# Optimization experiments

Measured on AMD Instinct MI355X. Metric: run time of the kernel, lower is better.

## Reference

```python
import jax, jax.numpy as jnp
import numpy as np

DIM = 384; H = 56; W = 56; WS = 7; SHIFT = 3; NH = 12; B = 32
N = WS * WS                 # 49 tokens per window
NW = (H // WS) * (W // WS)  # 64 windows per image
HD = DIM // NH
EPS = 1e-5


def _rel_coords_table():
    c = np.arange(-(WS - 1), WS, dtype=np.float32)
    hh, ww = np.meshgrid(c, c, indexing='ij')
    t = np.stack([hh, ww], -1)[None]          # (1, 2*WS-1, 2*WS-1, 2)
    t = t / (WS - 1) * 8.0
    t = np.sign(t) * np.log2(np.abs(t) + 1.0) / 3.0
    return t.astype(np.float32)


def _rel_pos_index():
    coords = np.stack(np.meshgrid(np.arange(WS), np.arange(WS), indexing='ij'))  # (2,WS,WS)
    cf = coords.reshape(2, -1)
    rc = (cf[:, :, None] - cf[:, None, :]).transpose(1, 2, 0)  # (N,N,2)
    rc[..., 0] += WS - 1
    rc[..., 1] += WS - 1
    rc[..., 0] *= 2 * WS - 1
    return rc.sum(-1)  # (N,N) int


def _attn_mask():
    img = np.zeros((H, W))
    sl = [slice(0, -WS), slice(-WS, -SHIFT), slice(-SHIFT, None)]
    cnt = 0
    for hs in sl:
        for ws in sl:
            img[hs, ws] = cnt
            cnt += 1
    mw = img.reshape(H // WS, WS, W // WS, WS).transpose(0, 2, 1, 3).reshape(-1, N)
    diff = mw[:, None, :] - mw[:, :, None]  # (NW, N, N)
    return np.where(diff != 0, -100.0, 0.0).astype(np.float32)


_RCT = jnp.asarray(_rel_coords_table())
_RPI = jnp.asarray(_rel_pos_index().reshape(-1))
_MASK = jnp.asarray(_attn_mask())


def _layernorm(x, g, b):
    mu = jnp.mean(x, -1, keepdims=True)
    var = jnp.mean(jnp.square(x - mu), -1, keepdims=True)
    return (x - mu) * jax.lax.rsqrt(var + EPS) * g + b


def _forward(x, qkv_w, q_bias, v_bias, logit_scale, cpb_w1, cpb_b1, cpb_w2,
             proj_w, proj_b, norm1_g, norm1_b, norm2_g, norm2_b,
             mlp_w1, mlp_b1, mlp_w2, mlp_b2):
    shortcut = x
    xg = x.reshape(B, H, W, DIM)
    xg = jnp.roll(xg, shift=(-SHIFT, -SHIFT), axis=(1, 2))
    # window partition -> (B*NW, N, C)
    xw = xg.reshape(B, H // WS, WS, W // WS, WS, DIM).transpose(0, 1, 3, 2, 4, 5)
    xw = xw.reshape(B * NW, N, DIM)

    qkv_bias = jnp.concatenate([q_bias, jnp.zeros_like(v_bias), v_bias])
    qkv = xw @ qkv_w.T + qkv_bias                       # (Bw, N, 3C)
    qkv = qkv.reshape(B * NW, N, 3, NH, HD).transpose(2, 0, 3, 1, 4)
    q, k, v = qkv[0], qkv[1], qkv[2]                    # (Bw, NH, N, HD)

    qn = q / jnp.maximum(jnp.linalg.norm(q, axis=-1, keepdims=True), 1e-12)
    kn = k / jnp.maximum(jnp.linalg.norm(k, axis=-1, keepdims=True), 1e-12)
    attn = jnp.einsum('whnd,whmd->whnm', qn, kn)        # cosine attention
    scale = jnp.exp(jnp.minimum(logit_scale, jnp.log(100.0)))  # (NH,1,1)
    attn = attn * scale

    # CPB-MLP relative position bias
    bt = jnp.maximum(_RCT @ cpb_w1.T + cpb_b1, 0.0) @ cpb_w2.T  # (1,13,13,NH)
    bt = bt.reshape(-1, NH)
    rel_bias = bt[_RPI].reshape(N, N, NH).transpose(2, 0, 1)    # (NH,N,N)
    rel_bias = 16.0 * jax.nn.sigmoid(rel_bias)
    attn = attn + rel_bias[None]

    attn = attn.reshape(B, NW, NH, N, N) + _MASK[None, :, None]
    attn = jax.nn.softmax(attn, axis=-1).reshape(B * NW, NH, N, N)

    out = jnp.einsum('whnm,whmd->whnd', attn, v)        # (Bw, NH, N, HD)
    out = out.transpose(0, 2, 1, 3).reshape(B * NW, N, DIM)
    out = out @ proj_w.T + proj_b

    # window reverse + un-shift
    xg = out.reshape(B, H // WS, W // WS, WS, WS, DIM).transpose(0, 1, 3, 2, 4, 5)
    xg = xg.reshape(B, H, W, DIM)
    xg = jnp.roll(xg, shift=(SHIFT, SHIFT), axis=(1, 2))
    attn_out = xg.reshape(B, H * W, DIM)

    # SwinV2 post-norm residuals
    x1 = shortcut + _layernorm(attn_out, norm1_g, norm1_b)
    h = jax.nn.gelu(x1 @ mlp_w1.T + mlp_b1, approximate=False) @ mlp_w2.T + mlp_b2
    return x1 + _layernorm(h, norm2_g, norm2_b)


def setup_inputs() -> dict:
    key = jax.random.key(0)
    ks = jax.random.split(key, 8)
    s = 0.02
    return {
        'x': jax.random.normal(ks[0], (B, H * W, DIM), jnp.float32),
        'qkv_w': jax.random.normal(ks[1], (3 * DIM, DIM), jnp.float32) * s,
        'q_bias': jnp.zeros((DIM,), jnp.float32),
        'v_bias': jnp.zeros((DIM,), jnp.float32),
        'logit_scale': jnp.log(10.0 * jnp.ones((NH, 1, 1), jnp.float32)),
        'cpb_w1': jax.random.normal(ks[2], (512, 2), jnp.float32) * s,
        'cpb_b1': jnp.zeros((512,), jnp.float32),
        'cpb_w2': jax.random.normal(ks[3], (NH, 512), jnp.float32) * s,
        'proj_w': jax.random.normal(ks[4], (DIM, DIM), jnp.float32) * s,
        'proj_b': jnp.zeros((DIM,), jnp.float32),
        'norm1_g': jnp.ones((DIM,), jnp.float32),
        'norm1_b': jnp.zeros((DIM,), jnp.float32),
        'norm2_g': jnp.ones((DIM,), jnp.float32),
        'norm2_b': jnp.zeros((DIM,), jnp.float32),
        'mlp_w1': jax.random.normal(ks[5], (4 * DIM, DIM), jnp.float32) * s,
        'mlp_b1': jnp.zeros((4 * DIM,), jnp.float32),
        'mlp_w2': jax.random.normal(ks[6], (DIM, 4 * DIM), jnp.float32) * s,
        'mlp_b2': jnp.zeros((DIM,), jnp.float32),
    }


def reference(x, qkv_w, q_bias, v_bias, logit_scale, cpb_w1, cpb_b1, cpb_w2,
              proj_w, proj_b, norm1_g, norm1_b, norm2_g, norm2_b,
              mlp_w1, mlp_b1, mlp_w2, mlp_b2):
    return _forward(x, qkv_w, q_bias, v_bias, logit_scale, cpb_w1, cpb_b1, cpb_w2,
                    proj_w, proj_b, norm1_g, norm1_b, norm2_g, norm2_b,
                    mlp_w1, mlp_b1, mlp_w2, mlp_b2)
```

## Files before the change

kernel.cpp:

```cpp
#include <hip/hip_runtime.h>
#include <hip/hip_bf16.h>
#include <math.h>

#define DIM 384
#define NH 12
#define HD 32
#define NWIN 2048
#define TOKENS 100352
#define NSTG 6

typedef unsigned short u16;
typedef unsigned int u32;
typedef __attribute__((ext_vector_type(8))) short bf16x8;
typedef __attribute__((ext_vector_type(4))) float f32x4;

__device__ __forceinline__ float b2f(u16 u){ return __uint_as_float(((u32)u) << 16); }
__device__ __forceinline__ u16 f2b(float f){
  u32 x = __float_as_uint(f);
  return (u16)((x + 0x7FFFu + ((x >> 16) & 1u)) >> 16);
}

__device__ __forceinline__ void gld16(void* lds, const void* g){
  __builtin_amdgcn_global_load_lds((const __attribute__((address_space(1))) u32*)g,
                                   (__attribute__((address_space(3))) u32*)lds, 16, 0, 0);
}

__global__ void k_wconv(const float* __restrict__ w1, const float* __restrict__ w2,
                        const float* __restrict__ qw, const float* __restrict__ pw,
                        u16* __restrict__ w1s, u16* __restrict__ w2s,
                        u16* __restrict__ qwbf, u16* __restrict__ pws){
  const int n12 = 1536*384, n3 = 1152*384, n4 = 384*384;
  for (int d = blockIdx.x*blockDim.x + threadIdx.x; d < n12; d += gridDim.x*blockDim.x){
    int tile = d >> 12, w = d & 4095;
    int rowl = w >> 5, g = (w >> 3) & 3, e = w & 7;
    int hci = tile / 12, rem = tile - hci*12;
    int kk = ((g ^ ((rowl >> 1) & 3)) << 3) + e;
    w1s[d] = f2b(w1[(size_t)(hci*128 + rowl)*384 + rem*32 + kk]);
    int ks = rem / 3, t = rem - ks*3;
    w2s[d] = f2b(w2[(size_t)(t*128 + rowl)*1536 + hci*128 + ks*32 + kk]);
    if (d < n3) qwbf[d] = f2b(qw[d]);
    if (d < n4){
      int pt = d >> 12, pwd = d & 4095;
      int prl = pwd >> 5, pg = (pwd >> 3) & 3, pe = pwd & 7;
      int pks = pt / 3, ptt = pt - pks*3;
      int pkk = ((pg ^ ((prl >> 1) & 3)) << 3) + pe;
      pws[d] = f2b(pw[(size_t)(ptt*128 + prl)*384 + pks*32 + pkk]);
    }
  }
}

__global__ void k_bias(const float* __restrict__ w1, const float* __restrict__ b1,
                       const float* __restrict__ w2, float* __restrict__ tab){
  __shared__ float hid[512];
  int e = blockIdx.x;
  int i = e / 13, j = e % 13;
  float t0 = (float)(i - 6) * (8.0f / 6.0f);
  float t1 = (float)(j - 6) * (8.0f / 6.0f);
  t0 = copysignf(log2f(fabsf(t0) + 1.f) * (1.f / 3.f), t0);
  t1 = copysignf(log2f(fabsf(t1) + 1.f) * (1.f / 3.f), t1);
  for (int jj = threadIdx.x; jj < 512; jj += blockDim.x)
    hid[jj] = fmaxf(w1[jj*2]*t0 + w1[jj*2+1]*t1 + b1[jj], 0.f);
  __syncthreads();
  if (threadIdx.x < 12){
    float s = 0.f;
    for (int jj = 0; jj < 512; ++jj) s += hid[jj] * w2[threadIdx.x*512 + jj];
    tab[e*12 + threadIdx.x] = s;
  }
}

__global__ void k_bias2(const float* __restrict__ tab, float* __restrict__ biasfull){
  int h = blockIdx.x;
  for (int e = threadIdx.x; e < 49*49; e += blockDim.x){
    int i = e / 49, j = e - (e/49)*49;
    int ih = i/7, iw = i - ih*7, jh = j/7, jw = j - jh*7;
    float bv = tab[((ih-jh+6)*13 + (iw-jw+6))*12 + h];
    biasfull[h*2401 + e] = 16.f / (1.f + expf(-bv));
  }
}

__device__ __forceinline__ void qkv_stage(
    int kc, char* Ad, char* Bd, const float* __restrict__ x, size_t asrc,
    bool arok, int ar, int aq, const u16* __restrict__ bbase, int tid){
  if (arok){
    float4 v4 = *(const float4*)(x + asrc + kc + aq*4);
    u16 p0=f2b(v4.x), p1=f2b(v4.y), p2=f2b(v4.z), p3=f2b(v4.w);
    *(uint2*)(Ad + ar*80 + aq*8) = (uint2){(u32)p0|((u32)p1<<16), (u32)p2|((u32)p3<<16)};
  } else {
    *(uint2*)(Ad + ar*80 + aq*8) = (uint2){0u, 0u};
  }
  #pragma unroll
  for (int i = 0; i < 3; ++i){
    int s = tid + i*512, n = s >> 2, g = s & 3;
    bf16x8 v = *(const bf16x8*)(bbase + (size_t)n*DIM + kc + (g ^ (n&3))*8);
    *(bf16x8*)(Bd + n*64 + g*16) = v;
  }
}

__global__ __launch_bounds__(512, 4) void k_qkv(
    const float* __restrict__ x, const u16* __restrict__ qkvbf,
    const float* __restrict__ q_bias, const float* __restrict__ v_bias,
    const float* __restrict__ logit_scale,
    u16* __restrict__ Qg, u16* __restrict__ Kg, u16* __restrict__ Vg){
  __shared__ __align__(16) char Ab[2][5120];
  __shared__ __align__(16) char Bb[2][24576];

  int tid = threadIdx.x;
  int lane = tid & 63, wid = tid >> 6;
  int l15 = lane & 15, lg = lane >> 4;
  int wm = wid >> 2, wn = wid & 3;
  int win = blockIdx.x, NT = blockIdx.y;
  int b = win >> 6, wi = win & 63, wh = wi >> 3, ww = wi & 7;

  int ar = tid >> 3, aq = tid & 7;
  bool arok = ar < 49;
  size_t asrc = 0;
  if (arok){
    int th = ar / 7, tw = ar - (ar/7)*7;
    int gh = wh*7 + th + 3; if (gh >= 56) gh -= 56;
    int gw = ww*7 + tw + 3; if (gw >= 56) gw -= 56;
    asrc = ((size_t)(b*3136 + gh*56 + gw))*DIM;
  }
  const u16* bbase = qkvbf + (size_t)NT*384*DIM;

  f32x4 acc[2][6];
  #pragma unroll
  for (int mf = 0; mf < 2; ++mf)
    #pragma unroll
    for (int nf = 0; nf < 6; ++nf) acc[mf][nf] = (f32x4){0.f,0.f,0.f,0.f};

  qkv_stage(0, Ab[0], Bb[0], x, asrc, arok, ar, aq, bbase, tid);
  __syncthreads();

  for (int t = 0; t < 12; ++t){
    int cur = t & 1;
    if (t < 11)
      qkv_stage((t+1)*32, Ab[cur^1], Bb[cur^1], x, asrc, arok, ar, aq, bbase, tid);
    bf16x8 af[2];
    #pragma unroll
    for (int mf = 0; mf < 2; ++mf){
      int row = wm*32 + mf*16 + l15;
      af[mf] = *(const bf16x8*)(Ab[cur] + row*80 + lg*16);
    }
    #pragma unroll
    for (int nf = 0; nf < 6; ++nf){
      int n = wn*96 + nf*16 + l15;
      bf16x8 bfv = *(const bf16x8*)(Bb[cur] + n*64 + ((lg ^ (n&3))*16));
      #pragma unroll
      for (int mf = 0; mf < 2; ++mf)
        acc[mf][nf] = __builtin_amdgcn_mfma_f32_16x16x32_bf16(af[mf], bfv, acc[mf][nf], 0, 0, 0);
    }
    __syncthreads();
  }

  if (NT == 0){
    #pragma unroll
    for (int p = 0; p < 3; ++p){
      int h = wn*3 + p;
      float qb0 = q_bias[h*32 + l15], qb1 = q_bias[h*32 + 16 + l15];
      float sc = __expf(fminf(logit_scale[h], 4.6051702f));
      #pragma unroll
      for (int mf = 0; mf < 2; ++mf)
        #pragma unroll
        for (int r = 0; r < 4; ++r){
          float a0 = acc[mf][2*p][r] + qb0;
          float a1 = acc[mf][2*p+1][r] + qb1;
          float sq = a0*a0 + a1*a1;
          #pragma unroll
          for (int off = 1; off < 16; off <<= 1) sq += __shfl_xor(sq, off, 64);
          float rq = sc / fmaxf(sqrtf(sq), 1e-12f);
          int grow = wm*32 + mf*16 + lg*4 + r;
          if (grow < 49){
            u16* dst = Qg + (size_t)win*18816 + h*1568 + grow*32;
            dst[l15]      = f2b(a0*rq);
            dst[16 + l15] = f2b(a1*rq);
          }
        }
    }
  } else if (NT == 1){
    #pragma unroll
    for (int p = 0; p < 3; ++p){
      int h = wn*3 + p;
      #pragma unroll
      for (int mf = 0; mf < 2; ++mf)
        #pragma unroll
        for (int r = 0; r < 4; ++r){
          float a0 = acc[mf][2*p][r], a1 = acc[mf][2*p+1][r];
          float sk = a0*a0 + a1*a1;
          #pragma unroll
          for (int off = 1; off < 16; off <<= 1) sk += __shfl_xor(sk, off, 64);
          float rk = 1.f / fmaxf(sqrtf(sk), 1e-12f);
          int grow = wm*32 + mf*16 + lg*4 + r;
          if (grow < 49){
            u16* dst = Kg + (size_t)win*18816 + h*1568 + grow*32;
            dst[l15]      = f2b(a0*rk);
            dst[16 + l15] = f2b(a1*rk);
          }
        }
    }
  } else {
    #pragma unroll
    for (int nf = 0; nf < 6; ++nf){
      int col = wn*96 + nf*16 + l15;
      int h = col >> 5, c = col & 31;
      float vb = v_bias[col];
      #pragma unroll
      for (int mf = 0; mf < 2; ++mf){
        int gbase = wm*32 + mf*16 + lg*4;
        u16* dst = Vg + (size_t)win*18816 + h*1568 + c;
        #pragma unroll
        for (int r = 0; r < 4; ++r){
          int grow = gbase + r;
          if (grow < 49) dst[grow*32] = f2b(acc[mf][nf][r] + vb);
        }
      }
    }
  }
}

__global__ __launch_bounds__(256, 3) void k_attn2(
    const u16* __restrict__ Qg, const u16* __restrict__ Kg, const u16* __restrict__ Vg,
    const float* __restrict__ biasfull, u16* __restrict__ outwin){
  __shared__ __align__(16) char pb[4][2304];

  int tid = threadIdx.x, lane = tid & 63, wid = tid >> 6;
  int l15 = lane & 15, lg = lane >> 4;
  int win = blockIdx.x;
  int wi = win & 63, wh = wi >> 3, ww = wi & 7;

  float mask16[4][4];
  int   bidx[4][4];
  #pragma unroll
  for (int nf = 0; nf < 4; ++nf){
    int j = nf*16 + l15;
    int j2 = j < 49 ? j : 48;
    int jh = j2/7, jw = j2 - jh*7;
    int ghj = wh*7+jh, gwj = ww*7+jw;
    int zj = (ghj<49?0:(ghj<53?1:2))*3 + (gwj<49?0:(gwj<53?1:2));
    #pragma unroll
    for (int r = 0; r < 4; ++r){
      int i = wid*16 + lg*4 + r;
      int i2 = i < 49 ? i : 48;
      int ih = i2/7, iw = i2 - ih*7;
      int ghi = wh*7+ih, gwi = ww*7+iw;
      int zi = (ghi<49?0:(ghi<53?1:2))*3 + (gwi<49?0:(gwi<53?1:2));
      mask16[nf][r] = (j < 49) ? (zi != zj ? -100.f : 0.f) : -1e30f;
      bidx[nf][r]   = i2*49 + j2;
    }
  }

  const u16* qwin = Qg + (size_t)win*18816;
  const u16* kwin = Kg + (size_t)win*18816;
  const u16* vwin = Vg + (size_t)win*18816;
  char* pbw = pb[wid];

  int arow = wid*16 + l15;
  int arc  = arow < 49 ? arow : 48;

  bf16x8 qa[12];
  #pragma unroll
  for (int h = 0; h < 12; ++h)
    qa[h] = *(const bf16x8*)(qwin + h*1568 + arc*32 + lg*8);
  __syncthreads();

  #pragma unroll
  for (int h = 0; h < 12; ++h){
    bf16x8 kb[4];
    #pragma unroll
    for (int nf = 0; nf < 4; ++nf){
      int j = nf*16 + l15; int j2 = j < 49 ? j : 48;
      kb[nf] = *(const bf16x8*)(kwin + h*1568 + j2*32 + lg*8);
    }
    bf16x8 vb0[2], vb1[2];
    #pragma unroll
    for (int ksp = 0; ksp < 2; ++ksp){
      #pragma unroll
      for (int tt = 0; tt < 8; ++tt){
        int j = ksp*32 + lg*8 + tt; int j2 = j < 49 ? j : 48;
        vb0[ksp][tt] = (short)vwin[h*1568 + j2*32 + l15];
        vb1[ksp][tt] = (short)vwin[h*1568 + j2*32 + 16 + l15];
      }
    }
    float bias16[4][4];
    #pragma unroll
    for (int nf = 0; nf < 4; ++nf)
      #pragma unroll
      for (int r = 0; r < 4; ++r)
        bias16[nf][r] = biasfull[h*2401 + bidx[nf][r]];
    f32x4 s[4];
    #pragma unroll
    for (int nf = 0; nf < 4; ++nf)
      s[nf] = __builtin_amdgcn_mfma_f32_16x16x32_bf16(qa[h], kb[nf],
                (f32x4){0.f,0.f,0.f,0.f}, 0, 0, 0);
    #pragma unroll
    for (int nf = 0; nf < 4; ++nf)
      #pragma unroll
      for (int r = 0; r < 4; ++r)
        s[nf][r] += bias16[nf][r] + mask16[nf][r];
    #pragma unroll
    for (int r = 0; r < 4; ++r){
      float m = fmaxf(fmaxf(s[0][r], s[1][r]), fmaxf(s[2][r], s[3][r]));
      #pragma unroll
      for (int off = 1; off < 16; off <<= 1) m = fmaxf(m, __shfl_xor(m, off, 64));
      float e0 = __expf(s[0][r]-m), e1 = __expf(s[1][r]-m);
      float e2 = __expf(s[2][r]-m), e3 = __expf(s[3][r]-m);
      float sum = e0+e1+e2+e3;
      #pragma unroll
      for (int off = 1; off < 16; off <<= 1) sum += __shfl_xor(sum, off, 64);
      float rs = 1.f/sum;
      s[0][r] = e0*rs; s[1][r] = e1*rs; s[2][r] = e2*rs; s[3][r] = e3*rs;
    }
    #pragma unroll
    for (int nf = 0; nf < 4; ++nf){
      int j = nf*16 + l15;
      #pragma unroll
      for (int r = 0; r < 4; ++r)
        *(u16*)(pbw + (lg*4+r)*144 + j*2) = f2b(s[nf][r]);
    }
    f32x4 o0 = (f32x4){0.f,0.f,0.f,0.f}, o1 = o0;
    #pragma unroll
    for (int ksp = 0; ksp < 2; ++ksp){
      bf16x8 pa = *(const bf16x8*)(pbw + l15*144 + ksp*64 + lg*16);
      o0 = __builtin_amdgcn_mfma_f32_16x16x32_bf16(pa, vb0[ksp], o0, 0, 0, 0);
      o1 = __builtin_amdgcn_mfma_f32_16x16x32_bf16(pa, vb1[ksp], o1, 0, 0, 0);
    }
    #pragma unroll
    for (int r = 0; r < 4; ++r){
      int row = wid*16 + lg*4 + r;
      if (row < 49){
        u16* dst = outwin + ((size_t)win*49 + row)*DIM + h*HD;
        dst[l15]      = f2b(o0[r]);
        dst[16 + l15] = f2b(o1[r]);
      }
    }
  }
}

__global__ __launch_bounds__(512, 2) void k_proj(
    const u16* __restrict__ outwin, const u16* __restrict__ pws,
    const float* __restrict__ proj_b, const float* __restrict__ x,
    const float* __restrict__ n1g, const float* __restrict__ n1b,
    float* __restrict__ x1){
  extern __shared__ char smem[];
  char* sb = smem;
  char* Wb = smem + 49152;

  int tid  = threadIdx.x;
  int lane = tid & 63, wid = tid >> 6;
  int l15  = lane & 15, lg = lane >> 4;
  int gt0 = blockIdx.x * 64;

  for (int e = tid; e < 64*48; e += 512){
    int r = e / 48, q8 = e - (e/48)*48;
    int gtok = gt0 + r;
    int b = gtok / 3136, r2 = gtok - b*3136;
    int oh = r2 / 56, ow = r2 - oh*56;
    int hs = oh + 53; if (hs >= 56) hs -= 56;
    int ws2 = ow + 53; if (ws2 >= 56) ws2 -= 56;
    int win = b*64 + (hs/7)*8 + (ws2/7);
    int row = (hs%7)*7 + (ws2%7);
    bf16x8 v = *(const bf16x8*)(outwin + ((size_t)win*49 + row)*DIM + q8*8);
    *(bf16x8*)(sb + r*768 + ((q8*16) ^ ((r&15)<<4))) = v;
  }

  f32x4 acc[4][3];
  #pragma unroll
  for (int mf = 0; mf < 4; ++mf)
    #pragma unroll
    for (int t = 0; t < 3; ++t){
      float pbv = proj_b[(wid + 8*t)*16 + l15];
      acc[mf][t] = (f32x4){pbv, pbv, pbv, pbv};
    }

  int goff = tid*16;
  int rowl = wid*16 + l15;
  int wswz = (lg ^ ((rowl >> 1) & 3)) << 4;
  #pragma unroll
  for (int sp = 0; sp < NSTG-1; ++sp)
    gld16(Wb + sp*8192 + wid*1024, (const char*)pws + (size_t)sp*8192 + goff);
  __syncthreads();

  #pragma unroll
  for (int ks = 0; ks < 12; ++ks){
    int k0 = ks*32 + lg*8;
    bf16x8 pa[4];
    #pragma unroll
    for (int mf = 0; mf < 4; ++mf){
      int row = mf*16 + l15;
      pa[mf] = *(const bf16x8*)(sb + row*768 + ((k0*2) ^ ((row&15)<<4)));
    }
    #pragma unroll
    for (int t = 0; t < 3; ++t){
      int st = ks*3 + t;
      asm volatile("s_waitcnt vmcnt(4)" ::: "memory");
      __builtin_amdgcn_sched_barrier(0);
      {
        int rp = st + 5;
        char* dst = Wb + ((st+5)%6)*8192 + wid*1024;
        if (rp < 36) gld16(dst, (const char*)pws + (size_t)rp*8192 + goff);
        else         gld16(dst, (const char*)pws + goff);
      }
      char* Wcur = Wb + (st%6)*8192;
      bf16x8 wv = *(const bf16x8*)(Wcur + rowl*64 + wswz);
      #pragma unroll
      for (int mf = 0; mf < 4; ++mf)
        acc[mf][t] = __builtin_amdgcn_mfma_f32_16x16x32_bf16(pa[mf], wv, acc[mf][t], 0, 0, 0);
    }
  }
  __syncthreads();

  float* part = (float*)Wb;
  float* lnf  = (float*)(Wb + 4096);
  float s1a[4][4], s2a[4][4];
  #pragma unroll
  for (int mf = 0; mf < 4; ++mf)
    #pragma unroll
    for (int r = 0; r < 4; ++r){
      float p1 = acc[mf][0][r] + acc[mf][1][r] + acc[mf][2][r];
      float p2 = acc[mf][0][r]*acc[mf][0][r] + acc[mf][1][r]*acc[mf][1][r]
               + acc[mf][2][r]*acc[mf][2][r];
      #pragma unroll
      for (int off = 1; off < 16; off <<= 1){
        p1 += __shfl_xor(p1, off, 64);
        p2 += __shfl_xor(p2, off, 64);
      }
      s1a[mf][r] = p1; s2a[mf][r] = p2;
    }
  if (l15 == 0){
    #pragma unroll
    for (int mf = 0; mf < 4; ++mf)
      #pragma unroll
      for (int r = 0; r < 4; ++r){
        int row = mf*16 + lg*4 + r;
        part[(row*8 + wid)*2]     = s1a[mf][r];
        part[(row*8 + wid)*2 + 1] = s2a[mf][r];
      }
  }
  __syncthreads();
  if (tid < 64){
    float t1 = 0.f, t2 = 0.f;
    #pragma unroll
    for (int w = 0; w < 8; ++w){
      t1 += part[(tid*8 + w)*2];
      t2 += part[(tid*8 + w)*2 + 1];
    }
    float mu = t1*(1.f/384.f);
    lnf[tid*2]     = mu;
    lnf[tid*2 + 1] = rsqrtf(t2*(1.f/384.f) - mu*mu + 1e-5f);
  }
  __syncthreads();
  #pragma unroll
  for (int mf = 0; mf < 4; ++mf)
    #pragma unroll
    for (int r = 0; r < 4; ++r){
      int row = mf*16 + lg*4 + r;
      float mu = lnf[row*2], rstd = lnf[row*2 + 1];
      #pragma unroll
      for (int t = 0; t < 3; ++t){
        int col = (wid + 8*t)*16 + l15;
        x1[(size_t)(gt0 + row)*DIM + col] =
            (acc[mf][t][r]-mu)*rstd*n1g[col] + n1b[col] + x[(size_t)(gt0 + row)*DIM + col];
      }
    }
}

__global__ __launch_bounds__(512, 4) void k_mlp(
    const float* __restrict__ x1, const u16* __restrict__ w1s, const float* __restrict__ b1,
    const u16* __restrict__ w2s, const float* __restrict__ b2,
    const float* __restrict__ n2g, const float* __restrict__ n2b,
    float* __restrict__ out){
  extern __shared__ char smem[];
  char* xb = smem;
  char* Wb = smem + 24576;
  char* hb = smem + 24576 + 49152;

  int tid  = threadIdx.x;
  int lane = tid & 63, wid = tid >> 6;
  int l15  = lane & 15, lg = lane >> 4;
  int gt0 = blockIdx.x * 32;

  for (int e = tid; e < 32*48; e += 512){
    int r = e / 48, q8 = e - (e/48)*48;
    const float4* src = (const float4*)(x1 + (size_t)(gt0+r)*DIM + q8*8);
    float4 a = src[0], c = src[1];
    bf16x8 v;
    v[0]=(short)f2b(a.x); v[1]=(short)f2b(a.y); v[2]=(short)f2b(a.z); v[3]=(short)f2b(a.w);
    v[4]=(short)f2b(c.x); v[5]=(short)f2b(c.y); v[6]=(short)f2b(c.z); v[7]=(short)f2b(c.w);
    *(bf16x8*)(xb + r*768 + ((q8*16) ^ ((r&15)<<4))) = v;
  }
  int b1c = wid*16 + l15;
  float b1r0 = b1[b1c],          b1r1 = b1[128 + b1c],  b1r2 = b1[256 + b1c];
  float b1r3 = b1[384 + b1c],    b1r4 = b1[512 + b1c],  b1r5 = b1[640 + b1c];
  float b1r6 = b1[768 + b1c],    b1r7 = b1[896 + b1c],  b1r8 = b1[1024 + b1c];
  float b1r9 = b1[1152 + b1c],   b1r10 = b1[1280 + b1c], b1r11 = b1[1408 + b1c];

  f32x4 acc2[2][3];
  #pragma unroll
  for (int mf = 0; mf < 2; ++mf)
    #pragma unroll
    for (int t = 0; t < 3; ++t){
      float bb = b2[(wid + 8*t)*16 + l15];
      acc2[mf][t] = (f32x4){bb, bb, bb, bb};
    }

  int goff = tid*16;
  int rowl = wid*16 + l15;
  int wswz = (lg ^ ((rowl >> 1) & 3)) << 4;
  #pragma unroll
  for (int sp = 0; sp < NSTG-1; ++sp)
    gld16(Wb + sp*8192 + wid*1024, (const char*)w1s + (size_t)sp*8192 + goff);
  __syncthreads();

  for (int hci = 0; hci < 12; ++hci){
    const char* w1c = (const char*)w1s + (size_t)hci*98304;
    const char* w2c = (const char*)w2s + (size_t)hci*98304;
    const char* w1n = (const char*)w1s + (size_t)(hci+1)*98304;

    float bb = hci==0?b1r0 : hci==1?b1r1 : hci==2?b1r2 : hci==3?b1r3 :
               hci==4?b1r4 : hci==5?b1r5 : hci==6?b1r6 : hci==7?b1r7 :
               hci==8?b1r8 : hci==9?b1r9 : hci==10?b1r10 : b1r11;
    f32x4 accH[2];
    #pragma unroll
    for (int mf = 0; mf < 2; ++mf) accH[mf] = (f32x4){bb, bb, bb, bb};

    #pragma unroll
    for (int ksp = 0; ksp < 12; ++ksp){
      asm volatile("s_waitcnt vmcnt(4)" ::: "memory");
      __builtin_amdgcn_sched_barrier(0);
      {
        int rp = ksp + 5;
        char* dst = Wb + ((ksp+5)%6)*8192 + wid*1024;
        const char* src = (rp < 12) ? (w1c + (size_t)rp*8192)
                                    : (w2c + (size_t)(rp-12)*8192);
        gld16(dst, src + goff);
      }
      char* Wcur = Wb + (ksp%6)*8192;
      int k0 = ksp*32 + lg*8;
      bf16x8 wfr = *(const bf16x8*)(Wcur + rowl*64 + wswz);
      bf16x8 afr[2];
      #pragma unroll
      for (int mf = 0; mf < 2; ++mf){
        int row = mf*16 + l15;
        afr[mf] = *(const bf16x8*)(xb + row*768 + ((k0*2) ^ ((row&15)<<4)));
      }
      #pragma unroll
      for (int mf = 0; mf < 2; ++mf)
        accH[mf] = __builtin_amdgcn_mfma_f32_16x16x32_bf16(afr[mf], wfr, accH[mf], 0, 0, 0);
    }

    #pragma unroll
    for (int mf = 0; mf < 2; ++mf)
      #pragma unroll
      for (int r = 0; r < 4; ++r){
        float v = accH[mf][r];
        float u = v*(1.f + 0.044715f*v*v);
        v = v * __builtin_amdgcn_rcpf(1.f + __expf(-1.5957691f*u));
        int row = mf*16 + lg*4 + r;
        int col = wid*16 + l15;
        *(u16*)(hb + row*256 + ((col*2) ^ ((row&15)<<4))) = f2b(v);
      }
    asm volatile("s_waitcnt lgkmcnt(0)" ::: "memory");
    __builtin_amdgcn_s_barrier();
    __builtin_amdgcn_sched_barrier(0);

    #pragma unroll
    for (int ks = 0; ks < 4; ++ks){
      int k0 = ks*32 + lg*8;
      bf16x8 pa[2];
      #pragma unroll
      for (int mf = 0; mf < 2; ++mf){
        int row = mf*16 + l15;
        pa[mf] = *(const bf16x8*)(hb + row*256 + ((k0*2) ^ ((row&15)<<4)));
      }
      #pragma unroll
      for (int t = 0; t < 3; ++t){
        int st = ks*3 + t;
        asm volatile("s_waitcnt vmcnt(4)" ::: "memory");
        __builtin_amdgcn_sched_barrier(0);
        {
          int rp = st + 17;
          char* dst = Wb + ((st+5)%6)*8192 + wid*1024;
          if (rp < 24)       gld16(dst, w2c + (size_t)(rp-12)*8192 + goff);
          else if (hci < 11) gld16(dst, w1n + (size_t)(rp-24)*8192 + goff);
          else               gld16(dst, (const char*)w1s + goff);
        }
        char* Wcur = Wb + (st%6)*8192;
        bf16x8 wv = *(const bf16x8*)(Wcur + rowl*64 + wswz);
        #pragma unroll
        for (int mf = 0; mf < 2; ++mf)
          acc2[mf][t] = __builtin_amdgcn_mfma_f32_16x16x32_bf16(pa[mf], wv, acc2[mf][t], 0, 0, 0);
      }
    }
    asm volatile("s_waitcnt lgkmcnt(0)" ::: "memory");
    __builtin_amdgcn_s_barrier();
    __builtin_amdgcn_sched_barrier(0);
  }
  __syncthreads();

  float* part = (float*)hb;
  float* lnf  = (float*)(hb + 2048);
  float s1a[2][4], s2a[2][4];
  #pragma unroll
  for (int mf = 0; mf < 2; ++mf)
    #pragma unroll
    for (int r = 0; r < 4; ++r){
      float p1 = acc2[mf][0][r] + acc2[mf][1][r] + acc2[mf][2][r];
      float p2 = acc2[mf][0][r]*acc2[mf][0][r] + acc2[mf][1][r]*acc2[mf][1][r]
               + acc2[mf][2][r]*acc2[mf][2][r];
      #pragma unroll
      for (int off = 1; off < 16; off <<= 1){
        p1 += __shfl_xor(p1, off, 64);
        p2 += __shfl_xor(p2, off, 64);
      }
      s1a[mf][r] = p1; s2a[mf][r] = p2;
    }
  if (l15 == 0){
    #pragma unroll
    for (int mf = 0; mf < 2; ++mf)
      #pragma unroll
      for (int r = 0; r < 4; ++r){
        int row = mf*16 + lg*4 + r;
        part[(row*8 + wid)*2]     = s1a[mf][r];
        part[(row*8 + wid)*2 + 1] = s2a[mf][r];
      }
  }
  __syncthreads();
  if (tid < 32){
    float t1 = 0.f, t2 = 0.f;
    #pragma unroll
    for (int w = 0; w < 8; ++w){
      t1 += part[(tid*8 + w)*2];
      t2 += part[(tid*8 + w)*2 + 1];
    }
    float mu = t1*(1.f/384.f);
    lnf[tid*2]     = mu;
    lnf[tid*2 + 1] = rsqrtf(t2*(1.f/384.f) - mu*mu + 1e-5f);
  }
  __syncthreads();
  #pragma unroll
  for (int mf = 0; mf < 2; ++mf)
    #pragma unroll
    for (int r = 0; r < 4; ++r){
      int row = mf*16 + lg*4 + r;
      float mu = lnf[row*2], rstd = lnf[row*2 + 1];
      #pragma unroll
      for (int t = 0; t < 3; ++t){
        int col = (wid + 8*t)*16 + l15;
        float resid = x1[(size_t)(gt0 + row)*DIM + col];
        out[(size_t)(gt0 + row)*DIM + col] =
            resid + (acc2[mf][t][r]-mu)*rstd*n2g[col] + n2b[col];
      }
    }
}

extern "C" void kernel_launch(void* const* d_in, const int* in_sizes, int n_in,
                              void* d_out, int out_size, void* d_ws, size_t ws_size,
                              hipStream_t stream){
  const float* x           = (const float*)d_in[0];
  const float* qkv_w       = (const float*)d_in[1];
  const float* q_bias      = (const float*)d_in[2];
  const float* v_bias      = (const float*)d_in[3];
  const float* logit_scale = (const float*)d_in[4];
  const float* cpb_w1      = (const float*)d_in[5];
  const float* cpb_b1      = (const float*)d_in[6];
  const float* cpb_w2      = (const float*)d_in[7];
  const float* proj_w      = (const float*)d_in[8];
  const float* proj_b      = (const float*)d_in[9];
  const float* n1g         = (const float*)d_in[10];
  const float* n1b         = (const float*)d_in[11];
  const float* n2g         = (const float*)d_in[12];
  const float* n2b         = (const float*)d_in[13];
  const float* mlp_w1      = (const float*)d_in[14];
  const float* mlp_b1      = (const float*)d_in[15];
  const float* mlp_w2      = (const float*)d_in[16];
  const float* mlp_b2      = (const float*)d_in[17];

  char* ws = (char*)d_ws;
  float* tab      = (float*)ws;
  float* biasfull = (float*)(ws + 8192);
  u16*  Qg     = (u16*)(ws + 126976);
  u16*  qkvbf  = (u16*)(ws + 126976 + 77070336ull);
  u16*  pws    = (u16*)(ws + 126976 + 77070336ull + 884736ull);
  u16*  w1s    = (u16*)(ws + 126976 + 77070336ull + 884736ull + 294912ull);
  u16*  w2s    = (u16*)(ws + 126976 + 77070336ull + 884736ull + 294912ull + 1179648ull);
  u16*  Kg     = (u16*)d_out;
  u16*  Vg     = Kg + (size_t)NWIN*18816;
  u16*  outwin = Qg;
  float* x1  = (float*)d_out;
  float* out = (float*)d_out;

  hipLaunchKernelGGL(k_bias, dim3(169), dim3(256), 0, stream, cpb_w1, cpb_b1, cpb_w2, tab);
  hipLaunchKernelGGL(k_bias2, dim3(12), dim3(256), 0, stream, tab, biasfull);
  hipLaunchKernelGGL(k_wconv, dim3(1024), dim3(256), 0, stream,
                     mlp_w1, mlp_w2, qkv_w, proj_w, w1s, w2s, qkvbf, pws);
  hipLaunchKernelGGL(k_qkv, dim3(NWIN, 3), dim3(512), 0, stream,
                     x, qkvbf, q_bias, v_bias, logit_scale, Qg, Kg, Vg);
  hipLaunchKernelGGL(k_attn2, dim3(NWIN), dim3(256), 0, stream,
                     Qg, Kg, Vg, biasfull, outwin);
  hipLaunchKernelGGL(k_proj, dim3(TOKENS/64), dim3(512), 98304, stream,
                     outwin, pws, proj_b, x, n1g, n1b, x1);
  hipLaunchKernelGGL(k_mlp, dim3(TOKENS/32), dim3(512), 81920, stream,
                     x1, w1s, mlp_b1, w2s, mlp_b2, n2g, n2b, out);
}
```

Baseline: 1.004 ms.

## Stage V through a double-buffered transposed LDS tile with next-head prefetch

The attention kernel used to gather V with 16 strided scalar global loads per lane per head. It now loads each head's V tile with coalesced 8-byte loads and scatters it transposed into an LDS buffer, so the MFMA B-operands become single vector LDS reads. The next head's V is prefetched into registers while the current head computes, using two LDS buffers. The cost is an extra __syncthreads per head and more LDS per block. Columns 49..55 of the transposed tile are never written, and vector reads run past the row width, so the fixed zero probabilities can meet uninitialised LDS data (NaN risk).

```diff
diff --git a/kernel.cpp b/kernel.cpp
--- a/kernel.cpp
+++ b/kernel.cpp
@@ -221,6 +221,7 @@
     const u16* __restrict__ Qg, const u16* __restrict__ Kg, const u16* __restrict__ Vg,
     const float* __restrict__ biasfull, u16* __restrict__ outwin){
   __shared__ __align__(16) char pb[4][2304];
+  __shared__ __align__(16) u16  vt[2][32][56];
 
   int tid = threadIdx.x, lane = tid & 63, wid = tid >> 6;
   int l15 = lane & 15, lg = lane >> 4;
@@ -260,25 +261,41 @@
   #pragma unroll
   for (int h = 0; h < 12; ++h)
     qa[h] = *(const bf16x8*)(qwin + h*1568 + arc*32 + lg*8);
+
+  {
+    uint2 v0 = (uint2){0u,0u}, v1 = (uint2){0u,0u};
+    if (tid < 392)       v0 = *(const uint2*)(vwin + tid*4);
+    if (tid + 256 < 392) v1 = *(const uint2*)(vwin + (tid+256)*4);
+    if (tid < 392){
+      int flat = tid*4, j = flat>>5, c = flat&31;
+      vt[0][c+0][j] = (u16)(v0.x & 0xffffu);
+      vt[0][c+1][j] = (u16)(v0.x >> 16);
+      vt[0][c+2][j] = (u16)(v0.y & 0xffffu);
+      vt[0][c+3][j] = (u16)(v0.y >> 16);
+    }
+    if (tid + 256 < 392){
+      int flat = (tid+256)*4, j = flat>>5, c = flat&31;
+      vt[0][c+0][j] = (u16)(v1.x & 0xffffu);
+      vt[0][c+1][j] = (u16)(v1.x >> 16);
+      vt[0][c+2][j] = (u16)(v1.y & 0xffffu);
+      vt[0][c+3][j] = (u16)(v1.y >> 16);
+    }
+  }
   __syncthreads();
 
   #pragma unroll
   for (int h = 0; h < 12; ++h){
+    uint2 nv0 = (uint2){0u,0u}, nv1 = (uint2){0u,0u};
+    if (h < 11){
+      const u16* vh = vwin + (h+1)*1568;
+      if (tid < 392)       nv0 = *(const uint2*)(vh + tid*4);
+      if (tid + 256 < 392) nv1 = *(const uint2*)(vh + (tid+256)*4);
+    }
     bf16x8 kb[4];
     #pragma unroll
     for (int nf = 0; nf < 4; ++nf){
       int j = nf*16 + l15; int j2 = j < 49 ? j : 48;
       kb[nf] = *(const bf16x8*)(kwin + h*1568 + j2*32 + lg*8);
-    }
-    bf16x8 vb0[2], vb1[2];
-    #pragma unroll
-    for (int ksp = 0; ksp < 2; ++ksp){
-      #pragma unroll
-      for (int tt = 0; tt < 8; ++tt){
-        int j = ksp*32 + lg*8 + tt; int j2 = j < 49 ? j : 48;
-        vb0[ksp][tt] = (short)vwin[h*1568 + j2*32 + l15];
-        vb1[ksp][tt] = (short)vwin[h*1568 + j2*32 + 16 + l15];
-      }
     }
     float bias16[4][4];
     #pragma unroll
@@ -320,8 +337,10 @@
     #pragma unroll
     for (int ksp = 0; ksp < 2; ++ksp){
       bf16x8 pa = *(const bf16x8*)(pbw + l15*144 + ksp*64 + lg*16);
-      o0 = __builtin_amdgcn_mfma_f32_16x16x32_bf16(pa, vb0[ksp], o0, 0, 0, 0);
-      o1 = __builtin_amdgcn_mfma_f32_16x16x32_bf16(pa, vb1[ksp], o1, 0, 0, 0);
+      bf16x8 vb0 = *(const bf16x8*)&vt[h&1][l15][ksp*32 + lg*8];
+      bf16x8 vb1 = *(const bf16x8*)&vt[h&1][16+l15][ksp*32 + lg*8];
+      o0 = __builtin_amdgcn_mfma_f32_16x16x32_bf16(pa, vb0, o0, 0, 0, 0);
+      o1 = __builtin_amdgcn_mfma_f32_16x16x32_bf16(pa, vb1, o1, 0, 0, 0);
     }
     #pragma unroll
     for (int r = 0; r < 4; ++r){
@@ -332,6 +351,23 @@
         dst[16 + l15] = f2b(o1[r]);
       }
     }
+    if (h < 11){
+      if (tid < 392){
+        int flat = tid*4, j = flat>>5, c = flat&31;
+        vt[(h+1)&1][c+0][j] = (u16)(nv0.x & 0xffffu);
+        vt[(h+1)&1][c+1][j] = (u16)(nv0.x >> 16);
+        vt[(h+1)&1][c+2][j] = (u16)(nv0.y & 0xffffu);
+        vt[(h+1)&1][c+3][j] = (u16)(nv0.y >> 16);
+      }
+      if (tid + 256 < 392){
+        int flat = (tid+256)*4, j = flat>>5, c = flat&31;
+        vt[(h+1)&1][c+0][j] = (u16)(nv1.x & 0xffffu);
+        vt[(h+1)&1][c+1][j] = (u16)(nv1.x >> 16);
+        vt[(h+1)&1][c+2][j] = (u16)(nv1.y & 0xffffu);
+        vt[(h+1)&1][c+3][j] = (u16)(nv1.y >> 16);
+      }
+    }
+    __syncthreads();
   }
 }
 
```

After: 1.014 ms. No clear change (+1.0%).
